# Kernel optimization log

Hardware: AMD Instinct MI355X
Metric: run time of the kernel (lower is better)

The kernel has to match this reference:

```python
import jax, jax.numpy as jnp
import numpy as np

COORD_DIM = 2
NUM_CHANNELS = 3
LATENT = 128
HIDDEN = 64
N0 = 8192
RADIUS = 0.035
RADII = (RADIUS, 2.0 * RADIUS)
ITER_COUNT = 3


def _radius_edges(y, x, r):
    # y: (Ny,d) source points, x: (Nx,d) query points -> edge lists (src into y, dst into x)
    d2 = ((x[:, None, :] - y[None, :, :]) ** 2).sum(-1)
    dst, src = np.nonzero(d2 <= r * r)
    return jnp.asarray(src, jnp.int32), jnp.asarray(dst, jnp.int32)


def setup_inputs():
    rng = np.random.default_rng(0)
    coords_np = rng.uniform(size=(COORD_DIM, N0)).astype(np.float32)
    c0 = coords_np.T            # (N0, d) fine level
    c1 = coords_np[:, ::2].T    # (N1, d) coarse level (stride-2 subsample)
    r_cross = max(RADII)
    e01_src, e01_dst = _radius_edges(c0, c1, r_cross)   # GK_0_1: y=lvl0, x=lvl1
    e10_src, e10_dst = _radius_edges(c1, c0, r_cross)   # GK_1_0: y=lvl1, x=lvl0
    e00_src, e00_dst = _radius_edges(c0, c0, RADII[0])  # GK_0_0
    e11_src, e11_dst = _radius_edges(c1, c1, RADII[1])  # GK_1_1

    key = jax.random.key(0)
    ks = iter(jax.random.split(key, 40))

    def lin(fi, fo):
        return jax.random.normal(next(ks), (fi, fo), jnp.float32) / np.float32(np.sqrt(fi))

    inp = dict(
        coords=jnp.asarray(coords_np),
        samples=jax.random.normal(next(ks), (N0, NUM_CHANNELS), jnp.float32),
        sigma=jax.random.uniform(next(ks), (1,), jnp.float32),
        fc_lift_w=lin(NUM_CHANNELS, LATENT), fc_lift_b=jnp.zeros((LATENT,), jnp.float32),
        fc_proj_w=lin(LATENT, NUM_CHANNELS), fc_proj_b=jnp.zeros((NUM_CHANNELS,), jnp.float32),
        W0_w=lin(LATENT, LATENT), W0_b=jnp.zeros((LATENT,), jnp.float32),
        W1_w=lin(LATENT, LATENT), W1_b=jnp.zeros((LATENT,), jnp.float32),
    )
    for name in ("gk00", "gk01", "gk10", "gk11"):
        inp[name + "_w1"] = lin(2 * COORD_DIM, HIDDEN)
        inp[name + "_b1"] = jnp.zeros((HIDDEN,), jnp.float32)
        inp[name + "_w2"] = lin(HIDDEN, LATENT)
        inp[name + "_b2"] = jnp.zeros((LATENT,), jnp.float32)
    inp.update(e00_src=e00_src, e00_dst=e00_dst, e01_src=e01_src, e01_dst=e01_dst,
               e10_src=e10_src, e10_dst=e10_dst, e11_src=e11_src, e11_dst=e11_dst)
    return inp


def _gno(xc, yc, f_y, src, dst, w1, b1, w2, b2, num_x):
    # gather -> edge kernel MLP on concat coords -> modulate by f_y -> scatter-mean
    e = jnp.concatenate([yc[src], xc[dst]], axis=1)        # (E, 2d)
    k = jax.nn.gelu(e @ w1 + b1) @ w2 + b2                 # (E, C) kernel values
    msg = k * f_y[src]                                     # 'linear' integral transform
    out = jax.ops.segment_sum(msg, dst, num_segments=num_x)
    cnt = jax.ops.segment_sum(jnp.ones(src.shape, msg.dtype), dst, num_segments=num_x)
    return out / jnp.maximum(cnt, 1.0)[:, None]


def reference(coords, samples, sigma,
              fc_lift_w, fc_lift_b, fc_proj_w, fc_proj_b,
              W0_w, W0_b, W1_w, W1_b,
              gk00_w1, gk00_b1, gk00_w2, gk00_b2,
              gk01_w1, gk01_b1, gk01_w2, gk01_b2,
              gk10_w1, gk10_b1, gk10_w2, gk10_b2,
              gk11_w1, gk11_b1, gk11_w2, gk11_b2,
              e00_src, e00_dst, e01_src, e01_dst,
              e10_src, e10_dst, e11_src, e11_dst):
    c0 = coords.T            # (N0, d)
    c1 = coords[:, ::2].T    # (N1, d)
    n0, n1 = c0.shape[0], c1.shape[0]
    v_down0 = samples @ fc_lift_w + fc_lift_b   # lifted features, never overwritten at level 0
    v_up0 = v_down0
    v_up1 = None
    for _ in range(ITER_COUNT):
        # downward pass (l = 1)
        vd = _gno(c1, c0, v_down0, e01_src, e01_dst, gk01_w1, gk01_b1, gk01_w2, gk01_b2, n1)
        if v_up1 is not None:
            vd = vd + v_up1
        v_down1 = jax.nn.relu(vd)
        # bottom level update
        v_up1 = jax.nn.relu(v_down1 @ W1_w + W1_b
                            + _gno(c1, c1, v_down1, e11_src, e11_dst, gk11_w1, gk11_b1, gk11_w2, gk11_b2, n1))
        # upward pass (l = 0)
        vu = _gno(c0, c1, v_up1, e10_src, e10_dst, gk10_w1, gk10_b1, gk10_w2, gk10_b2, n0)
        vu = vu + v_down0 @ W0_w + W0_b \
             + _gno(c0, c0, v_down0, e00_src, e00_dst, gk00_w1, gk00_b1, gk00_w2, gk00_b2, n0)
        v_up0 = jax.nn.relu(vu)
    return v_up0 @ fc_proj_w + fc_proj_b   # (N0, num_channels)
```

## Files before the change

kernel.cpp:

```cpp
#include <hip/hip_runtime.h>
#include <hip/hip_bf16.h>

typedef __attribute__((ext_vector_type(8))) short s8;
typedef __attribute__((ext_vector_type(4))) float f4;

#define TILE 128

__device__ __forceinline__ float gelu_fast(float x) {
    float x2 = x * x;
    float k  = x * fmaf(x2, 0.07135481624f, 1.59576912161f);
    float e  = __expf(k);
    float r  = __builtin_amdgcn_rcpf(e + 1.f);
    return x - x * r;
}

__device__ __forceinline__ short f2bf_bits(float v) {
    __hip_bfloat16 b = __float2bfloat16(v);
    return *(short*)&b;
}

struct RP { const int* edst; int E; int N; int* rowptr; };

__global__ void rowptr4_kernel(RP a, RP b, RP c, RP d) {
    RP g = (blockIdx.y == 0) ? a : (blockIdx.y == 1) ? b : (blockIdx.y == 2) ? c : d;
    int i = blockIdx.x * blockDim.x + threadIdx.x;
    if (i >= g.E) return;
    int dd = g.edst[i];
    int p  = (i == 0) ? -1 : g.edst[i - 1];
    for (int r = p + 1; r <= dd; ++r) g.rowptr[r] = i;
    if (i == g.E - 1)
        for (int r = dd + 1; r <= g.N; ++r) g.rowptr[r] = g.E;
}

__global__ __launch_bounds__(128) void pack_w2_kernel(
    const float* __restrict__ wa, const float* __restrict__ wb,
    const float* __restrict__ wc, const float* __restrict__ wd,
    short* __restrict__ out)
{
    const float* w2 = (blockIdx.x == 0) ? wa : (blockIdx.x == 1) ? wb
                    : (blockIdx.x == 2) ? wc : wd;
    short* dst = out + (size_t)blockIdx.x * 8192;
    const int t = threadIdx.x;
    const int w = t >> 6, lane = t & 63, q = (lane >> 4), n = lane & 15;
#pragma unroll
    for (int T = 0; T < 4; ++T)
#pragma unroll
        for (int s = 0; s < 2; ++s)
#pragma unroll
            for (int j = 0; j < 8; ++j) {
                int k  = s * 32 + q * 8 + j;
                int ch = 64 * w + 4 * n + T;
                dst[((((w * 4 + T) * 2 + s) * 64) + lane) * 8 + j] =
                    f2bf_bits(w2[k * 128 + ch]);
            }
}

struct GnoP {
    const float* fy;
    const int* esrc;
    const int* edst;
    const float* w1;
    const float* b1;
    const short* w2;
    const float* b2;
    float* acc;
    int E, sx, sy, pad;
};

__device__ __forceinline__ int seg_end(unsigned long long m0, unsigned long long m1, int a) {
    if (a < 64) {
        unsigned long long r = m0 >> a;
        if (r) return a + (int)__builtin_ctzll(r) + 1;
        return 64 + (int)__builtin_ctzll(m1) + 1;
    }
    unsigned long long r = m1 >> (a - 64);
    return a + (int)__builtin_ctzll(r) + 1;
}

__global__ __launch_bounds__(128) void gno_edge_kernel(
    const float* __restrict__ coords, int n0, GnoP A, GnoP B, int ntA)
{
    const GnoP P = (blockIdx.x < ntA) ? A : B;
    const int tile = (blockIdx.x < ntA) ? blockIdx.x : blockIdx.x - ntA;
    const int t = threadIdx.x;
    const int w = t >> 6, lane = t & 63, q = lane >> 4, n = lane & 15;
    const int e0 = tile * TILE;
    const int te = min(TILE, P.E - e0);

    __shared__ __align__(16) float s_crd[TILE][4];
    __shared__ int s_off[TILE];
    __shared__ int s_dst[TILE];
    __shared__ unsigned long long s_mask[2];
    __shared__ __align__(16) short s_gb[2][16 * 72];

    {
        int e = min(e0 + t, P.E - 1);
        int sv = P.esrc[e];
        int dv = P.edst[e];
        s_off[t] = sv * 128;
        s_dst[t] = dv;
        s_crd[t][0] = coords[(long)sv * P.sy];
        s_crd[t][1] = coords[n0 + (long)sv * P.sy];
        s_crd[t][2] = coords[(long)dv * P.sx];
        s_crd[t][3] = coords[n0 + (long)dv * P.sx];
    }

    const float rw0 = P.w1[lane], rw1v = P.w1[64 + lane];
    const float rwx = P.w1[128 + lane], rwy = P.w1[192 + lane], rb1 = P.b1[lane];
    s8 bfrag[4][2];
    const s8* w2f = (const s8*)P.w2;
#pragma unroll
    for (int T = 0; T < 4; ++T)
#pragma unroll
        for (int s = 0; s < 2; ++s)
            bfrag[T][s] = w2f[((w * 4 + T) * 2 + s) * 64 + lane];
    const f4 b2c = *(const f4*)&P.b2[w * 64 + 4 * n];

    __syncthreads();

    {
        int idx = w * 64 + lane;
        bool fl = (idx < te) && (idx == te - 1 || s_dst[idx + 1] != s_dst[idx]);
        unsigned long long m = __ballot(fl);
        if (lane == 0) s_mask[w] = m;
    }
    __syncthreads();
    const unsigned long long m0 = s_mask[0], m1 = s_mask[1];

    int g0 = 0;
    int b = seg_end(m0, m1, 0);
    f4 fvc[4];
#pragma unroll
    for (int r = 0; r < 4; ++r) {
        int row = q * 4 + r;
        if (row < b) fvc[r] = *(const f4*)&P.fy[(long)s_off[row] + w * 64 + 4 * n];
        else { f4 z = {0.f, 0.f, 0.f, 0.f}; fvc[r] = z; }
    }
    f4 accr = {0.f, 0.f, 0.f, 0.f};
    int gbp = 0;

    while (true) {
        int gn = g0 + 16, bn = b;
        const bool endseg = (gn >= b);
        if (endseg) { gn = b; if (gn < te) bn = seg_end(m0, m1, gn); }
        f4 fvn[4];
        if (gn < te) {
#pragma unroll
            for (int r = 0; r < 4; ++r) {
                int row = gn + q * 4 + r;
                if (row < bn) fvn[r] = *(const f4*)&P.fy[(long)s_off[row] + w * 64 + 4 * n];
                else { f4 z = {0.f, 0.f, 0.f, 0.f}; fvn[r] = z; }
            }
        }
#pragma unroll
        for (int i = 0; i < 8; ++i) {
            int j = 2 * i + w;
            int p = min(g0 + j, te - 1);
            const f4 crd = *(const f4*)s_crd[p];
            float x = fmaf(crd.x, rw0, fmaf(crd.y, rw1v,
                      fmaf(crd.z, rwx, fmaf(crd.w, rwy, rb1))));
            s_gb[gbp][j * 72 + lane] = f2bf_bits(gelu_fast(x));
        }
        __syncthreads();
        const s8 a0 = *(const s8*)&s_gb[gbp][n * 72 + q * 8];
        const s8 a1 = *(const s8*)&s_gb[gbp][n * 72 + q * 8 + 32];
        f4 c[4];
#pragma unroll
        for (int T = 0; T < 4; ++T) {
            f4 z = {0.f, 0.f, 0.f, 0.f};
            z = __builtin_amdgcn_mfma_f32_16x16x32_bf16(a0, bfrag[T][0], z, 0, 0, 0);
            c[T] = __builtin_amdgcn_mfma_f32_16x16x32_bf16(a1, bfrag[T][1], z, 0, 0, 0);
        }
#pragma unroll
        for (int r = 0; r < 4; ++r)
#pragma unroll
            for (int T = 0; T < 4; ++T)
                accr[T] += (c[T][r] + b2c[T]) * fvc[r][T];
        if (endseg) {
            const int dcur = s_dst[g0];
#pragma unroll
            for (int T = 0; T < 4; ++T) {
                float v = accr[T];
                v += __shfl_xor(v, 16, 64);
                v += __shfl_xor(v, 32, 64);
                if (q == 0)
                    atomicAdd(&P.acc[(long)dcur * 128 + w * 64 + 4 * n + T], v);
            }
            f4 z = {0.f, 0.f, 0.f, 0.f};
            accr = z;
        }
        if (gn >= te) break;
        g0 = gn; b = bn;
#pragma unroll
        for (int r = 0; r < 4; ++r) fvc[r] = fvn[r];
        gbp ^= 1;
    }
}

__global__ void zero_kernel(float* __restrict__ p, long n) {
    long i = ((long)blockIdx.x * 256 + threadIdx.x) * 4;
    if (i < n) { f4 z = {0.f, 0.f, 0.f, 0.f}; *(f4*)&p[i] = z; }
}

__global__ __launch_bounds__(256) void epi0001_kernel(
    float* __restrict__ acc, const int* __restrict__ rp00, int N0,
    const int* __restrict__ rp01, float* __restrict__ vd0zero, long ntot)
{
    long idx = (long)blockIdx.x * 256 + threadIdx.x;
    if (idx >= ntot) return;
    int d = (int)(idx >> 7);
    float deg;
    if (d < N0) { deg = (float)(rp00[d + 1] - rp00[d]); vd0zero[idx] = 0.f; }
    else        { deg = (float)(rp01[d - N0 + 1] - rp01[d - N0]); }
    acc[idx] = acc[idx] / fmaxf(deg, 1.f);
}

__global__ __launch_bounds__(128) void relu_mm_kernel(
    const float* __restrict__ base, float* __restrict__ accu,
    const int* __restrict__ rowptr, float* __restrict__ w1t,
    const float* __restrict__ W, const float* __restrict__ bias,
    float* __restrict__ vout, float* __restrict__ zbuf, int R)
{
    const int r0 = blockIdx.x * 8;
    const int t = threadIdx.x;
    __shared__ float s_x[8 * 128];
#pragma unroll
    for (int j = 0; j < 8; ++j) {
        int r = r0 + j;
        long o = (long)r * 128 + t;
        float v = base[o];
        if (accu) {
            float deg = (float)(rowptr[r + 1] - rowptr[r]);
            float u = fmaxf(accu[o] / fmaxf(deg, 1.f) + w1t[o], 0.f);
            v += u;
            accu[o] = 0.f;
        } else if (zbuf) {
            zbuf[o] = 0.f;
        }
        v = fmaxf(v, 0.f);
        s_x[j * 128 + t] = v;
        vout[o] = v;
    }
    __syncthreads();
    float acc[8];
    const float bc = bias[t];
#pragma unroll
    for (int j = 0; j < 8; ++j) acc[j] = bc;
    for (int hh = 0; hh < 128; ++hh) {
        float wv = W[hh * 128 + t];
#pragma unroll
        for (int j = 0; j < 8; ++j) acc[j] += s_x[j * 128 + hh] * wv;
    }
#pragma unroll
    for (int j = 0; j < 8; ++j)
        w1t[(long)(r0 + j) * 128 + t] = acc[j];
}

__global__ __launch_bounds__(256) void epi11_kernel(
    float* __restrict__ acc, const int* __restrict__ rowptr,
    const float* __restrict__ w1t, int N)
{
    long idx = (long)blockIdx.x * 256 + threadIdx.x;
    if (idx >= (long)N * 128) return;
    int d = (int)(idx >> 7);
    float deg = (float)(rowptr[d + 1] - rowptr[d]);
    acc[idx] = fmaxf(acc[idx] / fmaxf(deg, 1.f) + w1t[idx], 0.f);
}

__global__ __launch_bounds__(128) void lift_mm_kernel(
    const float* __restrict__ samples, const float* __restrict__ LW,
    const float* __restrict__ Lb, const float* __restrict__ W0,
    const float* __restrict__ W0b, float* __restrict__ vout,
    float* __restrict__ w0t, int R)
{
    const int r0 = blockIdx.x * 8;
    const int t = threadIdx.x;
    __shared__ float s_x[8 * 128];
#pragma unroll
    for (int j = 0; j < 8; ++j) {
        int r = r0 + j;
        float s0 = samples[r * 3 + 0], s1 = samples[r * 3 + 1], s2 = samples[r * 3 + 2];
        float v = s0 * LW[t] + s1 * LW[128 + t] + s2 * LW[256 + t] + Lb[t];
        s_x[j * 128 + t] = v;
        vout[(long)r * 128 + t] = v;
    }
    __syncthreads();
    float acc[8];
    const float bc = W0b[t];
#pragma unroll
    for (int j = 0; j < 8; ++j) acc[j] = bc;
    for (int hh = 0; hh < 128; ++hh) {
        float wv = W0[hh * 128 + t];
#pragma unroll
        for (int j = 0; j < 8; ++j) acc[j] += s_x[j * 128 + hh] * wv;
    }
#pragma unroll
    for (int j = 0; j < 8; ++j)
        w0t[(long)(r0 + j) * 128 + t] = acc[j];
}

__global__ __launch_bounds__(128) void epi_proj_kernel(
    const float* __restrict__ acc, const int* __restrict__ rowptr,
    const float* __restrict__ add0, const float* __restrict__ add1,
    const float* __restrict__ projw, const float* __restrict__ projb,
    float* __restrict__ fout, int N)
{
    const int d = blockIdx.x, t = threadIdx.x;
    float deg = (float)(rowptr[d + 1] - rowptr[d]);
    long o = (long)d * 128 + t;
    float res = fmaxf(acc[o] / fmaxf(deg, 1.f) + add0[o] + add1[o], 0.f);
    float p0 = res * projw[t * 3 + 0];
    float p1 = res * projw[t * 3 + 1];
    float p2 = res * projw[t * 3 + 2];
#pragma unroll
    for (int off = 32; off > 0; off >>= 1) {
        p0 += __shfl_down(p0, off);
        p1 += __shfl_down(p1, off);
        p2 += __shfl_down(p2, off);
    }
    __shared__ float sred[6];
    if ((t & 63) == 0) { int w = t >> 6; sred[w * 3 + 0] = p0; sred[w * 3 + 1] = p1; sred[w * 3 + 2] = p2; }
    __syncthreads();
    if (t < 3) fout[d * 3 + t] = sred[t] + sred[3 + t] + projb[t];
}

extern "C" void kernel_launch(void* const* d_in, const int* in_sizes, int n_in,
                              void* d_out, int out_size, void* d_ws, size_t ws_size,
                              hipStream_t stream)
{
    const float* coords  = (const float*)d_in[0];
    const float* samples = (const float*)d_in[1];
    const float* lift_w  = (const float*)d_in[3];
    const float* lift_b  = (const float*)d_in[4];
    const float* proj_w  = (const float*)d_in[5];
    const float* proj_b  = (const float*)d_in[6];
    const float* W0_w    = (const float*)d_in[7];
    const float* W0_b    = (const float*)d_in[8];
    const float* W1_w    = (const float*)d_in[9];
    const float* W1_b    = (const float*)d_in[10];
    const float *gw1[4], *gb1[4], *gw2[4], *gb2[4];
    for (int g = 0; g < 4; ++g) {
        gw1[g] = (const float*)d_in[11 + 4 * g + 0];
        gb1[g] = (const float*)d_in[11 + 4 * g + 1];
        gw2[g] = (const float*)d_in[11 + 4 * g + 2];
        gb2[g] = (const float*)d_in[11 + 4 * g + 3];
    }
    const int* es[4]; const int* ed[4]; int E[4];
    for (int g = 0; g < 4; ++g) {
        es[g] = (const int*)d_in[27 + 2 * g];
        ed[g] = (const int*)d_in[27 + 2 * g + 1];
        E[g]  = in_sizes[27 + 2 * g];
    }

    const int N0 = in_sizes[0] / 2;
    const int N1 = (N0 + 1) / 2;

    float* ws = (float*)d_ws;
    float* v_down0 = ws;
    float* w0term  = v_down0 + (size_t)N0 * 128;
    float* gno00o  = w0term  + (size_t)N0 * 128;
    float* gno01b  = gno00o  + (size_t)N0 * 128;
    float* v_down1 = gno01b  + (size_t)N1 * 128;
    float* w1term  = v_down1 + (size_t)N1 * 128;
    float* v_up1   = w1term  + (size_t)N1 * 128;
    short* w2pack  = (short*)(v_up1 + (size_t)N1 * 128);
    int*   rp      = (int*)(w2pack + 4 * 8192);
    int* rp00 = rp;
    int* rp01 = rp00 + (N0 + 1);
    int* rp10 = rp01 + (N1 + 1);
    int* rp11 = rp10 + (N0 + 1);

    {
        int maxE = E[0];
        for (int g = 1; g < 4; ++g) maxE = max(maxE, E[g]);
        RP a = {ed[0], E[0], N0, rp00};
        RP b = {ed[1], E[1], N1, rp01};
        RP c = {ed[2], E[2], N0, rp10};
        RP d = {ed[3], E[3], N1, rp11};
        dim3 grid((maxE + 255) / 256, 4);
        rowptr4_kernel<<<grid, 256, 0, stream>>>(a, b, c, d);
    }
    pack_w2_kernel<<<4, 128, 0, stream>>>(gw2[0], gw2[1], gw2[2], gw2[3], w2pack);

    const long n00 = (long)N0 * 128, n11 = (long)N1 * 128;

    zero_kernel<<<(int)((n00 + n11) / 4 + 255) / 256, 256, 0, stream>>>(gno00o, n00 + n11);
    lift_mm_kernel<<<N0 / 8, 128, 0, stream>>>(samples, lift_w, lift_b, W0_w, W0_b,
                                               v_down0, w0term, N0);

    GnoP P00 = {v_down0, es[0], ed[0], gw1[0], gb1[0], w2pack + 0 * 8192, gb2[0], gno00o, E[0], 1, 1, 0};
    GnoP P01 = {v_down0, es[1], ed[1], gw1[1], gb1[1], w2pack + 1 * 8192, gb2[1], gno01b, E[1], 2, 1, 0};
    GnoP P11 = {v_down1, es[3], ed[3], gw1[3], gb1[3], w2pack + 3 * 8192, gb2[3], v_up1,  E[3], 2, 2, 0};
    GnoP P10 = {v_up1,   es[2], ed[2], gw1[2], gb1[2], w2pack + 2 * 8192, gb2[2], v_down0, E[2], 1, 2, 0};

    {
        int tA = (E[0] + TILE - 1) / TILE, tB = (E[1] + TILE - 1) / TILE;
        gno_edge_kernel<<<tA + tB, 128, 0, stream>>>(coords, N0, P00, P01, tA);
    }
    epi0001_kernel<<<(int)((n00 + n11) + 255) / 256, 256, 0, stream>>>(
        gno00o, rp00, N0, rp01, v_down0, n00 + n11);

    for (int it = 0; it < 3; ++it) {
        relu_mm_kernel<<<N1 / 8, 128, 0, stream>>>(
            gno01b, (it == 0) ? nullptr : v_up1, rp11, w1term, W1_w, W1_b,
            v_down1, (it == 0) ? v_up1 : nullptr, N1);
        int tt = (E[3] + TILE - 1) / TILE;
        gno_edge_kernel<<<tt, 128, 0, stream>>>(coords, N0, P11, P11, tt);
    }
    epi11_kernel<<<(int)(n11 + 255) / 256, 256, 0, stream>>>(v_up1, rp11, w1term, N1);

    {
        int tt = (E[2] + TILE - 1) / TILE;
        gno_edge_kernel<<<tt, 128, 0, stream>>>(coords, N0, P10, P10, tt);
    }
    epi_proj_kernel<<<N0, 128, 0, stream>>>(v_down0, rp10, w0term, gno00o,
                                            proj_w, proj_b, (float*)d_out, N0);
}
```

Before: 379.6 us.

## Tighten GNO edge kernel: packed bf16 GELU, bias in MFMA, reordered prefetch

```diff
diff --git a/kernel.cpp b/kernel.cpp
--- a/kernel.cpp
+++ b/kernel.cpp
@@ -8,10 +8,15 @@
 
 __device__ __forceinline__ float gelu_fast(float x) {
     float x2 = x * x;
-    float k  = x * fmaf(x2, 0.07135481624f, 1.59576912161f);
-    float e  = __expf(k);
+    float k2 = x * fmaf(x2, 0.10294326f, 2.30220819f);
+    float e  = __builtin_amdgcn_exp2f(k2);
     float r  = __builtin_amdgcn_rcpf(e + 1.f);
-    return x - x * r;
+    return fmaf(-x, r, x);
+}
+
+__device__ __forceinline__ unsigned pack_bf16x2(float a, float b) {
+    __hip_bfloat162 h = __float22bfloat162_rn(make_float2(a, b));
+    return *(unsigned*)&h;
 }
 
 __device__ __forceinline__ short f2bf_bits(float v) {
@@ -37,22 +42,20 @@
     const float* __restrict__ wc, const float* __restrict__ wd,
     short* __restrict__ out)
 {
-    const float* w2 = (blockIdx.x == 0) ? wa : (blockIdx.x == 1) ? wb
-                    : (blockIdx.x == 2) ? wc : wd;
-    short* dst = out + (size_t)blockIdx.x * 8192;
+    const int g = blockIdx.x >> 2, T = blockIdx.x & 3;
+    const float* w2 = (g == 0) ? wa : (g == 1) ? wb : (g == 2) ? wc : wd;
+    short* dst = out + (size_t)g * 8192;
     const int t = threadIdx.x;
     const int w = t >> 6, lane = t & 63, q = (lane >> 4), n = lane & 15;
 #pragma unroll
-    for (int T = 0; T < 4; ++T)
-#pragma unroll
-        for (int s = 0; s < 2; ++s)
-#pragma unroll
-            for (int j = 0; j < 8; ++j) {
-                int k  = s * 32 + q * 8 + j;
-                int ch = 64 * w + 4 * n + T;
-                dst[((((w * 4 + T) * 2 + s) * 64) + lane) * 8 + j] =
-                    f2bf_bits(w2[k * 128 + ch]);
-            }
+    for (int s = 0; s < 2; ++s)
+#pragma unroll
+        for (int j = 0; j < 8; ++j) {
+            int k  = s * 32 + q * 8 + j;
+            int ch = 64 * w + 4 * n + T;
+            dst[((((w * 4 + T) * 2 + s) * 64) + lane) * 8 + j] =
+                f2bf_bits(w2[k * 128 + ch]);
+        }
 }
 
 struct GnoP {
@@ -87,7 +90,7 @@
     const int e0 = tile * TILE;
     const int te = min(TILE, P.E - e0);
 
-    __shared__ __align__(16) float s_crd[TILE][4];
+    __shared__ __align__(16) float s_crd[(TILE + 16) * 4];
     __shared__ int s_off[TILE];
     __shared__ int s_dst[TILE];
     __shared__ unsigned long long s_mask[2];
@@ -99,14 +102,19 @@
         int dv = P.edst[e];
         s_off[t] = sv * 128;
         s_dst[t] = dv;
-        s_crd[t][0] = coords[(long)sv * P.sy];
-        s_crd[t][1] = coords[n0 + (long)sv * P.sy];
-        s_crd[t][2] = coords[(long)dv * P.sx];
-        s_crd[t][3] = coords[n0 + (long)dv * P.sx];
-    }
-
-    const float rw0 = P.w1[lane], rw1v = P.w1[64 + lane];
-    const float rwx = P.w1[128 + lane], rwy = P.w1[192 + lane], rb1 = P.b1[lane];
+        f4 c4 = {coords[(long)sv * P.sy], coords[n0 + (long)sv * P.sy],
+                 coords[(long)dv * P.sx], coords[n0 + (long)dv * P.sx]};
+        *(f4*)&s_crd[t * 4] = c4;
+        if (t < 16) *(f4*)&s_crd[(TILE + t) * 4] = c4;
+    }
+
+    const int h0 = 2 * (lane & 31);
+    const float wA0 = P.w1[h0],       wA1 = P.w1[h0 + 1];
+    const float wB0 = P.w1[64 + h0],  wB1 = P.w1[65 + h0];
+    const float wC0 = P.w1[128 + h0], wC1 = P.w1[129 + h0];
+    const float wD0 = P.w1[192 + h0], wD1 = P.w1[193 + h0];
+    const float b10 = P.b1[h0],       b11 = P.b1[h0 + 1];
+
     s8 bfrag[4][2];
     const s8* w2f = (const s8*)P.w2;
 #pragma unroll
@@ -115,6 +123,11 @@
         for (int s = 0; s < 2; ++s)
             bfrag[T][s] = w2f[((w * 4 + T) * 2 + s) * 64 + lane];
     const f4 b2c = *(const f4*)&P.b2[w * 64 + 4 * n];
+    f4 b2i[4];
+#pragma unroll
+    for (int T = 0; T < 4; ++T) { f4 z = {b2c[T], b2c[T], b2c[T], b2c[T]}; b2i[T] = z; }
+
+    const float* fyl = P.fy + (w * 64 + 4 * n);
 
     __syncthreads();
 
@@ -133,33 +146,23 @@
 #pragma unroll
     for (int r = 0; r < 4; ++r) {
         int row = q * 4 + r;
-        if (row < b) fvc[r] = *(const f4*)&P.fy[(long)s_off[row] + w * 64 + 4 * n];
+        if (row < b) fvc[r] = *(const f4*)&fyl[s_off[row]];
         else { f4 z = {0.f, 0.f, 0.f, 0.f}; fvc[r] = z; }
     }
     f4 accr = {0.f, 0.f, 0.f, 0.f};
     int gbp = 0;
+    const int jh = lane >> 5;
 
     while (true) {
-        int gn = g0 + 16, bn = b;
-        const bool endseg = (gn >= b);
-        if (endseg) { gn = b; if (gn < te) bn = seg_end(m0, m1, gn); }
-        f4 fvn[4];
-        if (gn < te) {
-#pragma unroll
-            for (int r = 0; r < 4; ++r) {
-                int row = gn + q * 4 + r;
-                if (row < bn) fvn[r] = *(const f4*)&P.fy[(long)s_off[row] + w * 64 + 4 * n];
-                else { f4 z = {0.f, 0.f, 0.f, 0.f}; fvn[r] = z; }
-            }
-        }
-#pragma unroll
-        for (int i = 0; i < 8; ++i) {
-            int j = 2 * i + w;
-            int p = min(g0 + j, te - 1);
-            const f4 crd = *(const f4*)s_crd[p];
-            float x = fmaf(crd.x, rw0, fmaf(crd.y, rw1v,
-                      fmaf(crd.z, rwx, fmaf(crd.w, rwy, rb1))));
-            s_gb[gbp][j * 72 + lane] = f2bf_bits(gelu_fast(x));
+#pragma unroll
+        for (int i = 0; i < 4; ++i) {
+            int j = 4 * i + 2 * jh + w;
+            const f4 crd = *(const f4*)&s_crd[(g0 + j) * 4];
+            float x0 = fmaf(crd[0], wA0, fmaf(crd[1], wB0,
+                       fmaf(crd[2], wC0, fmaf(crd[3], wD0, b10))));
+            float x1 = fmaf(crd[0], wA1, fmaf(crd[1], wB1,
+                       fmaf(crd[2], wC1, fmaf(crd[3], wD1, b11))));
+            *(unsigned*)&s_gb[gbp][j * 72 + h0] = pack_bf16x2(gelu_fast(x0), gelu_fast(x1));
         }
         __syncthreads();
         const s8 a0 = *(const s8*)&s_gb[gbp][n * 72 + q * 8];
@@ -167,16 +170,20 @@
         f4 c[4];
 #pragma unroll
         for (int T = 0; T < 4; ++T) {
-            f4 z = {0.f, 0.f, 0.f, 0.f};
-            z = __builtin_amdgcn_mfma_f32_16x16x32_bf16(a0, bfrag[T][0], z, 0, 0, 0);
+            f4 z = __builtin_amdgcn_mfma_f32_16x16x32_bf16(a0, bfrag[T][0], b2i[T], 0, 0, 0);
             c[T] = __builtin_amdgcn_mfma_f32_16x16x32_bf16(a1, bfrag[T][1], z, 0, 0, 0);
         }
 #pragma unroll
         for (int r = 0; r < 4; ++r)
 #pragma unroll
             for (int T = 0; T < 4; ++T)
-                accr[T] += (c[T][r] + b2c[T]) * fvc[r][T];
+                accr[T] = fmaf(c[T][r], fvc[r][T], accr[T]);
+
+        int gn = g0 + 16, bn = b;
+        const bool endseg = (gn >= b);
         if (endseg) {
+            gn = b;
+            if (gn < te) bn = seg_end(m0, m1, gn);
             const int dcur = s_dst[g0];
 #pragma unroll
             for (int T = 0; T < 4; ++T) {
@@ -190,9 +197,13 @@
             accr = z;
         }
         if (gn >= te) break;
+#pragma unroll
+        for (int r = 0; r < 4; ++r) {
+            int row = gn + q * 4 + r;
+            if (row < bn) fvc[r] = *(const f4*)&fyl[s_off[row]];
+            else { f4 z = {0.f, 0.f, 0.f, 0.f}; fvc[r] = z; }
+        }
         g0 = gn; b = bn;
-#pragma unroll
-        for (int r = 0; r < 4; ++r) fvc[r] = fvn[r];
         gbp ^= 1;
     }
 }
@@ -246,6 +257,7 @@
     const float bc = bias[t];
 #pragma unroll
     for (int j = 0; j < 8; ++j) acc[j] = bc;
+#pragma unroll 4
     for (int hh = 0; hh < 128; ++hh) {
         float wv = W[hh * 128 + t];
 #pragma unroll
@@ -289,6 +301,7 @@
     const float bc = W0b[t];
 #pragma unroll
     for (int j = 0; j < 8; ++j) acc[j] = bc;
+#pragma unroll 4
     for (int hh = 0; hh < 128; ++hh) {
         float wv = W0[hh * 128 + t];
 #pragma unroll
@@ -380,7 +393,7 @@
         dim3 grid((maxE + 255) / 256, 4);
         rowptr4_kernel<<<grid, 256, 0, stream>>>(a, b, c, d);
     }
-    pack_w2_kernel<<<4, 128, 0, stream>>>(gw2[0], gw2[1], gw2[2], gw2[3], w2pack);
+    pack_w2_kernel<<<16, 128, 0, stream>>>(gw2[0], gw2[1], gw2[2], gw2[3], w2pack);
 
     const long n00 = (long)N0 * 128, n11 = (long)N1 * 128;
 
```

Result: faster. 356.5 us (-6.1%).
